# Optimization experiments

Hardware: AMD Instinct MI355X
Metric: run time of the kernel (lower is better)

The kernel has to match this reference:

```python
import jax, jax.numpy as jnp
import numpy as np

N = 40000   # nodes
E = 640000  # edges
D = 128     # hidden_dim
EPS = 1e-5  # LayerNorm eps


def setup_inputs() -> dict:
    key = jax.random.key(0)
    ks = jax.random.split(key, 18)
    s = 0.02
    inp = {
        "h": jax.random.normal(ks[0], (N, D), jnp.float32),
        "x": jax.random.normal(ks[1], (N, 3), jnp.float32),
        "edge_index": jax.random.randint(ks[2], (2, E), 0, N, jnp.int64 if jax.config.jax_enable_x64 else jnp.int32),
        "vel": jax.random.normal(ks[3], (N, 3), jnp.float32),
        # phi_e: Linear(2D+1 -> D), SiLU, Linear(D -> D), SiLU
        "We1": jax.random.normal(ks[4], (2 * D + 1, D), jnp.float32) * s,
        "be1": jnp.zeros((D,), jnp.float32),
        "We2": jax.random.normal(ks[5], (D, D), jnp.float32) * s,
        "be2": jnp.zeros((D,), jnp.float32),
        # phi_x: Linear(D -> D), SiLU, Linear(D -> 1)
        "Wx1": jax.random.normal(ks[6], (D, D), jnp.float32) * s,
        "bx1": jnp.zeros((D,), jnp.float32),
        "Wx2": jax.random.normal(ks[7], (D, 1), jnp.float32) * s,
        "bx2": jnp.zeros((1,), jnp.float32),
        # phi_h: Linear(2D -> D), SiLU, Linear(D -> D)
        "Wh1": jax.random.normal(ks[8], (2 * D, D), jnp.float32) * s,
        "bh1": jnp.zeros((D,), jnp.float32),
        "Wh2": jax.random.normal(ks[9], (D, D), jnp.float32) * s,
        "bh2": jnp.zeros((D,), jnp.float32),
        # LayerNorm
        "gamma": jnp.ones((D,), jnp.float32),
        "beta": jnp.zeros((D,), jnp.float32),
    }
    return inp


def reference(h, x, edge_index, vel,
              We1, be1, We2, be2,
              Wx1, bx1, Wx2, bx2,
              Wh1, bh1, Wh2, bh2,
              gamma, beta):
    src, dst = edge_index[0], edge_index[1]
    rel = x[src] - x[dst]                                  # [E,3]
    dist2 = jnp.sum(rel * rel, axis=-1, keepdims=True)     # [E,1]
    # note: original also computes dist/r_hat and vel[src] but never uses them

    # phi_e on edge features
    e_in = jnp.concatenate([h[src], h[dst], dist2], axis=-1)   # [E,2D+1]
    m = jax.nn.silu(e_in @ We1 + be1)
    m = jax.nn.silu(m @ We2 + be2)                             # [E,D]

    # coordinate update: scatter_mean of rel * phi_x(m) over dst
    coord_w = jax.nn.silu(m @ Wx1 + bx1) @ Wx2 + bx2           # [E,1]
    num = jax.ops.segment_sum(rel * coord_w, dst, num_segments=N)  # [N,3]
    cnt = jax.ops.segment_sum(jnp.ones((E, 1), x.dtype), dst, num_segments=N)
    x_new = x + num / jnp.maximum(cnt, 1.0)

    # node update: scatter_add of messages then phi_h + residual + LayerNorm
    agg = jax.ops.segment_sum(m, dst, num_segments=N)          # [N,D]
    upd = jax.nn.silu(jnp.concatenate([h, agg], axis=-1) @ Wh1 + bh1) @ Wh2 + bh2
    hn = h + upd
    mu = jnp.mean(hn, axis=-1, keepdims=True)
    var = jnp.var(hn, axis=-1, keepdims=True)
    h_out = (hn - mu) / jnp.sqrt(var + EPS) * gamma + beta
    return h_out, x_new
```

## Files before the change

kernel.cpp:

```cpp
#include <hip/hip_runtime.h>
#include <hip/hip_fp16.h>

#define NN 40000
#define NE 640000
#define DD 128
#define NW (NE/64)

typedef _Float16 half8 __attribute__((ext_vector_type(8)));
typedef float f32x4 __attribute__((ext_vector_type(4)));

__device__ __forceinline__ float silu_f(float x){
  return x * __builtin_amdgcn_rcpf(1.f + __expf(-x));
}

__device__ __forceinline__ half8 cvt_h8(float4 a, float4 b){
  half8 r;
  r[0]=(_Float16)a.x; r[1]=(_Float16)a.y; r[2]=(_Float16)a.z; r[3]=(_Float16)a.w;
  r[4]=(_Float16)b.x; r[5]=(_Float16)b.y; r[6]=(_Float16)b.z; r[7]=(_Float16)b.w;
  return r;
}

__device__ __forceinline__ void atom_pk_f16(_Float16* p, unsigned v){
  asm volatile("global_atomic_pk_add_f16 %0, %1, off" :: "v"(p), "v"(v));
}

__global__ void k_hist(const int* __restrict__ ei, int* __restrict__ counts,
                       uint4* __restrict__ aggz){
  int e = blockIdx.x*256 + threadIdx.x;
  if (e < NE){
    atomicAdd(&counts[ei[NE + e]], 1);
    aggz[e] = make_uint4(0,0,0,0);
  }
}

__global__ __launch_bounds__(1024)
void k_scanA(const int* __restrict__ counts, int* __restrict__ woff,
             int* __restrict__ bsum){
  __shared__ int wsum[16];
  const int tid = threadIdx.x, lane = tid & 63, wv = tid >> 6;
  int i = blockIdx.x*1024 + tid;
  int v = (i < NN) ? counts[i] : 0;
  int s = v;
  #pragma unroll
  for (int d = 1; d < 64; d <<= 1){
    int t = __shfl_up(s, d, 64);
    if (lane >= d) s += t;
  }
  if (lane == 63) wsum[wv] = s;
  __syncthreads();
  if (tid < 16){
    int t = wsum[tid];
    #pragma unroll
    for (int d = 1; d < 16; d <<= 1){
      int u = __shfl_up(t, d, 64);
      if (tid >= d) t += u;
    }
    wsum[tid] = t;
  }
  __syncthreads();
  int wbase = (wv == 0) ? 0 : wsum[wv-1];
  if (i < NN) woff[i] = wbase + s - v;
  if (tid == 1023) bsum[blockIdx.x] = wbase + s;
}

__global__ __launch_bounds__(1024)
void k_scanC(int* __restrict__ woff, const int* __restrict__ bsum){
  const int lane = threadIdx.x & 63;
  int v = (lane < 40) ? bsum[lane] : 0;
  int s = v;
  #pragma unroll
  for (int d = 1; d < 64; d <<= 1){
    int t = __shfl_up(s, d, 64);
    if (lane >= d) s += t;
  }
  int boff = (blockIdx.x == 0) ? 0 : __shfl(s, blockIdx.x - 1, 64);
  int i = blockIdx.x*1024 + threadIdx.x;
  if (i < NN) woff[i] += boff;
}

__global__ void k_scatter(const int* __restrict__ ei, int* __restrict__ woff,
                          unsigned* __restrict__ sdp){
  int e = blockIdx.x*256 + threadIdx.x;
  if (e < NE){
    int s = ei[e];
    int d = ei[NE + e];
    int p = atomicAdd(&woff[d], 1);
    sdp[p] = ((unsigned)s << 16) | (unsigned)d;
  }
}

__global__ void k_wt(const float* __restrict__ We1, const float* __restrict__ Wh1,
                     const float* __restrict__ Wh2,
                     _Float16* __restrict__ We1t, _Float16* __restrict__ Wh1t,
                     _Float16* __restrict__ Wh2t, int* __restrict__ counts){
  int i = blockIdx.x*256 + threadIdx.x;
  if (i < 128*256){
    int ch = i >> 8, k = i & 255;
    We1t[i] = (_Float16)We1[k*128 + ch];
    Wh1t[i] = (_Float16)Wh1[k*128 + ch];
  }
  if (i < 128*128){
    int ch = i >> 7, k = i & 127;
    Wh2t[i] = (_Float16)Wh2[k*128 + ch];
  }
  for (int c = i; c < NN; c += 32768) counts[c] = 0;
}

__global__ __launch_bounds__(256) __attribute__((amdgpu_waves_per_eu(3,4)))
void k_gpre(const float* __restrict__ h, const _Float16* __restrict__ We1t,
            const float* __restrict__ be1,
            _Float16* __restrict__ g1, _Float16* __restrict__ g2)
{
  const int tid = threadIdx.x, lane = tid & 63, w = tid >> 6;
  const int q = lane & 15, g = lane >> 4;
  const int base = (blockIdx.x*4 + w) * 16;
  float be1r[8];
  #pragma unroll
  for (int nt=0; nt<8; nt++) be1r[nt] = be1[nt*16+q];

  half8 a[4];
  #pragma unroll
  for (int kk=0; kk<4; kk++){
    const float* rp = h + (size_t)(base+q)*DD + kk*32 + g*8;
    a[kk] = cvt_h8(*(const float4*)rp, *(const float4*)(rp+4));
  }
  f32x4 ac1[8] = {}, ac2[8] = {};
  #pragma unroll
  for (int kk=0; kk<4; kk++){
    #pragma unroll
    for (int nt=0; nt<8; nt++){
      half8 b1 = *(const half8*)&We1t[(nt*16+q)*256 + kk*32 + g*8];
      half8 b2 = *(const half8*)&We1t[(nt*16+q)*256 + 128 + kk*32 + g*8];
      ac1[nt] = __builtin_amdgcn_mfma_f32_16x16x32_f16(a[kk], b1, ac1[nt], 0,0,0);
      ac2[nt] = __builtin_amdgcn_mfma_f32_16x16x32_f16(a[kk], b2, ac2[nt], 0,0,0);
    }
  }
  #pragma unroll
  for (int r=0;r<4;r++){
    int node = base + 4*g + r;
    #pragma unroll
    for (int nt=0; nt<8; nt++){
      g1[(size_t)node*DD + nt*16+q] = (_Float16)(ac1[nt][r] + be1r[nt]);
      g2[(size_t)node*DD + nt*16+q] = (_Float16)ac2[nt][r];
    }
  }
}

__global__ __launch_bounds__(1024) __attribute__((amdgpu_waves_per_eu(4,4)))
void egnn_edge(const _Float16* __restrict__ g1, const _Float16* __restrict__ g2,
               const float* __restrict__ x,
               const unsigned* __restrict__ sdp,
               const float* __restrict__ We1,
               const float* __restrict__ We2, const float* __restrict__ be2,
               const float* __restrict__ Wx1, const float* __restrict__ bx1,
               const float* __restrict__ Wx2, const float* __restrict__ bx2,
               _Float16* __restrict__ agg, float* __restrict__ cwb)
{
  __shared__ __align__(16) _Float16 W2t[128*128];
  __shared__ __align__(16) _Float16 Wxt[128*128];
  __shared__ __align__(16) _Float16 mbuf[16][16*128];
  __shared__ __align__(16) _Float16 w1l_lds[128];

  const int tid = threadIdx.x;
  for (int i = tid; i < 128*128; i += 1024){
    int ch = i & 127, k = i >> 7;
    int sw = (ch & 15) << 3;
    W2t[ch*128 + (k ^ sw)] = (_Float16)We2[k*128 + ch];
    Wxt[ch*128 + (k ^ sw)] = (_Float16)Wx1[k*128 + ch];
  }
  if (tid < 128) w1l_lds[tid] = (_Float16)We1[256*128 + tid];
  const int lane = tid & 63;
  const int w    = tid >> 6;
  const int q    = lane & 15;
  const int g    = lane >> 4;
  float be2r[8], bx1r[8], wx2r[8];
  #pragma unroll
  for (int nt = 0; nt < 8; nt++){
    int ch = nt*16 + q;
    be2r[nt] = be2[ch];
    bx1r[nt] = bx1[ch];
    wx2r[nt] = Wx2[ch];
  }
  const float bx2s = bx2[0];
  _Float16* mb = mbuf[w];
  __syncthreads();

  const int gw = blockIdx.x*16 + w;

  half8 w1l_h[4];
  #pragma unroll
  for (int kk=0; kk<4; kk++)
    w1l_h[kk] = *(const half8*)&w1l_lds[kk*32 + g*8];

  const unsigned sv = sdp[gw*64 + lane];
  const int esrc = (int)(sv >> 16);
  const int edst = (int)(sv & 0xffffu);
  float r0 = x[esrc*3+0] - x[edst*3+0];
  float r1 = x[esrc*3+1] - x[edst*3+1];
  float r2 = x[esrc*3+2] - x[edst*3+2];
  float d2 = r0*r0 + r1*r1 + r2*r2;

  const int first_dst = __shfl(edst, 0, 64);
  const int last_dst  = __shfl(edst, 63, 64);
  const bool prev_spill = (gw > 0)    && ((int)(sdp[gw*64 - 1] & 0xffffu) == first_dst);
  const bool next_spill = (gw < NW-1) && ((int)(sdp[gw*64 + 64] & 0xffffu) == last_dst);

  int srcq[4], dstq[4];
  __half2 d2h[4];
  #pragma unroll
  for (int mt=0; mt<4; mt++){
    srcq[mt] = __shfl(esrc, mt*16 + q, 64);
    dstq[mt] = __shfl(edst, mt*16 + q, 64);
    d2h[mt]  = __float2half2_rn(__shfl(d2, mt*16 + q, 64));
  }
  const __half2 one2 = __float2half2_rn(1.f);

  float fa0 = 0.f, fa1 = 0.f;
  int   fdprev = first_dst;
  bool  seg_first = true;

  uint4 pa1[4], pb1[4];
  #pragma unroll
  for (int kk=0; kk<4; kk++)
    pa1[kk] = *(const uint4*)(g1 + (size_t)srcq[0]*DD + kk*32 + g*8);

  #pragma unroll
  for (int mt=0; mt<4; mt++){
    uint4 (&cu1)[4] = (mt&1) ? pb1 : pa1;
    uint4 (&nu1)[4] = (mt&1) ? pa1 : pb1;
    if (mt < 3){
      #pragma unroll
      for (int kk=0; kk<4; kk++)
        nu1[kk] = *(const uint4*)(g1 + (size_t)srcq[mt+1]*DD + kk*32 + g*8);
    }

    half8 a[4];
    #pragma unroll
    for (int kk=0; kk<4; kk++){
      uint4 cu2 = *(const uint4*)(g2 + (size_t)dstq[mt]*DD + kk*32 + g*8);
      uint4 w4 = __builtin_bit_cast(uint4, w1l_h[kk]);
      unsigned uu1[4] = {cu1[kk].x, cu1[kk].y, cu1[kk].z, cu1[kk].w};
      unsigned uu2[4] = {cu2.x, cu2.y, cu2.z, cu2.w};
      unsigned ww[4]  = {w4.x, w4.y, w4.z, w4.w};
      unsigned zz[4];
      #pragma unroll
      for (int p2=0; p2<4; p2++){
        __half2 z = __hadd2(__builtin_bit_cast(__half2, uu1[p2]),
                            __builtin_bit_cast(__half2, uu2[p2]));
        z = __hfma2(d2h[mt], __builtin_bit_cast(__half2, ww[p2]), z);
        __half2 e   = h2exp(__hneg2(z));
        __half2 den = __hadd2(e, one2);
        __half2 m   = __hmul2(z, h2rcp(den));
        zz[p2] = __builtin_bit_cast(unsigned, m);
      }
      uint4 t; t.x = zz[0]; t.y = zz[1]; t.z = zz[2]; t.w = zz[3];
      a[kk] = __builtin_bit_cast(half8, t);
    }

    f32x4 acc2[8] = {};
    #pragma unroll
    for (int kk=0; kk<4; kk++){
      #pragma unroll
      for (int nt=0; nt<8; nt++){
        half8 b = *(const half8*)&W2t[(nt*16+q)*128 + ((kk*32+g*8) ^ (q<<3))];
        acc2[nt] = __builtin_amdgcn_mfma_f32_16x16x32_f16(a[kk], b, acc2[nt], 0,0,0);
      }
    }
    #pragma unroll
    for (int nt=0; nt<8; nt++){
      #pragma unroll
      for (int r=0;r<4;r++){
        float s = silu_f(acc2[nt][r] + be2r[nt]);
        int el = 4*g + r;
        mb[el*128 + ((nt*16+q) ^ (el<<3))] = (_Float16)s;
      }
    }
    f32x4 acc3[8] = {};
    #pragma unroll
    for (int kk=0; kk<4; kk++){
      half8 am = *(const half8*)&mb[q*128 + ((kk*32+g*8) ^ (q<<3))];
      #pragma unroll
      for (int nt=0; nt<8; nt++){
        half8 b = *(const half8*)&Wxt[(nt*16+q)*128 + ((kk*32+g*8) ^ (q<<3))];
        acc3[nt] = __builtin_amdgcn_mfma_f32_16x16x32_f16(am, b, acc3[nt], 0,0,0);
      }
    }
    float part[4] = {0.f,0.f,0.f,0.f};
    #pragma unroll
    for (int nt=0; nt<8; nt++){
      #pragma unroll
      for (int r=0;r<4;r++)
        part[r] += silu_f(acc3[nt][r] + bx1r[nt]) * wx2r[nt];
    }
    #pragma unroll
    for (int m=1; m<16; m<<=1){
      #pragma unroll
      for (int r=0;r<4;r++) part[r] += __shfl_xor(part[r], m, 64);
    }
    {
      float cw = part[0];
      if (q==1) cw = part[1]; else if (q==2) cw = part[2]; else if (q==3) cw = part[3];
      if (q < 4) cwb[gw*64 + mt*16 + 4*g + q] = cw + bx2s;
    }
    {
      unsigned mv[16];
      #pragma unroll
      for (int e2=0; e2<16; e2++)
        mv[e2] = *(const unsigned*)&mb[e2*128 + ((2*lane) ^ (e2<<3))];
      int dv[16];
      #pragma unroll
      for (int e2=0; e2<16; e2++) dv[e2] = __shfl(edst, mt*16 + e2, 64);
      #pragma unroll
      for (int e2=0; e2<16; e2++){
        if (dv[e2] != fdprev){
          __half2 hv; hv.x = __float2half(fa0); hv.y = __float2half(fa1);
          _Float16* p = agg + (size_t)fdprev*DD + 2*lane;
          if (seg_first && prev_spill) atom_pk_f16(p, __builtin_bit_cast(unsigned, hv));
          else                         *(__half2*)p = hv;
          fa0 = 0.f; fa1 = 0.f; fdprev = dv[e2]; seg_first = false;
        }
        __half2 mvv = __builtin_bit_cast(__half2, mv[e2]);
        fa0 += __half2float(mvv.x);
        fa1 += __half2float(mvv.y);
      }
    }
  }
  {
    __half2 hv; hv.x = __float2half(fa0); hv.y = __float2half(fa1);
    _Float16* p = agg + (size_t)fdprev*DD + 2*lane;
    if ((seg_first && prev_spill) || next_spill) atom_pk_f16(p, __builtin_bit_cast(unsigned, hv));
    else                                         *(__half2*)p = hv;
  }
}

__global__ __launch_bounds__(256) __attribute__((amdgpu_waves_per_eu(3,4)))
void egnn_node(const float* __restrict__ h, const _Float16* __restrict__ agg,
               const _Float16* __restrict__ Wh1t, const _Float16* __restrict__ Wh2t,
               const float* __restrict__ bh1, const float* __restrict__ bh2,
               const float* __restrict__ gam, const float* __restrict__ bet,
               float* __restrict__ hout)
{
  __shared__ __align__(16) _Float16 mbuf[4][16*128];
  const int tid = threadIdx.x, lane = tid & 63, w = tid >> 6;
  const int q = lane & 15, g = lane >> 4;
  const int base = (blockIdx.x*4 + w) * 16;
  float bh1r[8], bh2r[8], gr[8], br[8];
  #pragma unroll
  for (int nt=0; nt<8; nt++){
    int ch = nt*16+q;
    bh1r[nt]=bh1[ch]; bh2r[nt]=bh2[ch]; gr[nt]=gam[ch]; br[nt]=bet[ch];
  }
  _Float16* mb = mbuf[w];

  f32x4 ac1[8] = {};
  #pragma unroll
  for (int kk=0; kk<8; kk++){
    half8 a;
    if (kk < 4){
      const float* rp = h + (size_t)(base+q)*DD + kk*32 + g*8;
      a = cvt_h8(*(const float4*)rp, *(const float4*)(rp+4));
    } else {
      a = *(const half8*)(agg + (size_t)(base+q)*DD + (kk-4)*32 + g*8);
    }
    #pragma unroll
    for (int nt=0; nt<8; nt++){
      half8 b = *(const half8*)&Wh1t[(nt*16+q)*256 + kk*32 + g*8];
      ac1[nt] = __builtin_amdgcn_mfma_f32_16x16x32_f16(a, b, ac1[nt], 0,0,0);
    }
  }
  #pragma unroll
  for (int nt=0; nt<8; nt++){
    #pragma unroll
    for (int r=0;r<4;r++){
      float s = silu_f(ac1[nt][r] + bh1r[nt]);
      int el = 4*g + r;
      mb[el*128 + ((nt*16+q) ^ (el<<3))] = (_Float16)s;
    }
  }
  f32x4 ac2[8] = {};
  #pragma unroll
  for (int kk=0; kk<4; kk++){
    half8 am = *(const half8*)&mb[q*128 + ((kk*32+g*8) ^ (q<<3))];
    #pragma unroll
    for (int nt=0; nt<8; nt++){
      half8 b = *(const half8*)&Wh2t[(nt*16+q)*128 + kk*32 + g*8];
      ac2[nt] = __builtin_amdgcn_mfma_f32_16x16x32_f16(am, b, ac2[nt], 0,0,0);
    }
  }
  #pragma unroll
  for (int r=0;r<4;r++){
    int node = base + 4*g + r;
    float hv[8]; float s1=0.f, s2=0.f;
    #pragma unroll
    for (int nt=0; nt<8; nt++){
      float v = ac2[nt][r] + bh2r[nt] + h[(size_t)node*DD + nt*16 + q];
      hv[nt]=v; s1 += v; s2 += v*v;
    }
    #pragma unroll
    for (int m=1;m<16;m<<=1){ s1 += __shfl_xor(s1,m,64); s2 += __shfl_xor(s2,m,64); }
    float mu  = s1 * (1.f/128.f);
    float var = s2 * (1.f/128.f) - mu*mu;
    float rs  = rsqrtf(var + 1e-5f);
    #pragma unroll
    for (int nt=0; nt<8; nt++)
      hout[(size_t)node*DD + nt*16 + q] = (hv[nt]-mu)*rs*gr[nt] + br[nt];
  }
}

__global__ __launch_bounds__(256)
void k_coord(const float* __restrict__ x, const float* __restrict__ cwb,
             const unsigned* __restrict__ sdp, const int* __restrict__ counts,
             const int* __restrict__ woff, float* __restrict__ xout)
{
  const int tid = threadIdx.x, lane = tid & 63, w = tid >> 6;
  const int sub = lane >> 4, j0 = lane & 15;
  const int n = (blockIdx.x*4 + w)*4 + sub;
  if (n >= NN) return;
  const int cnt = counts[n];
  const int s = woff[n] - cnt;
  float xd0 = x[n*3+0], xd1 = x[n*3+1], xd2 = x[n*3+2];
  float s0=0.f, s1=0.f, s2=0.f;
  for (int j = j0; j < cnt; j += 16){
    int e = s + j;
    float cw = cwb[e];
    int src = (int)(sdp[e] >> 16);
    s0 += (x[src*3+0]-xd0)*cw;
    s1 += (x[src*3+1]-xd1)*cw;
    s2 += (x[src*3+2]-xd2)*cw;
  }
  #pragma unroll
  for (int m=1; m<16; m<<=1){
    s0 += __shfl_xor(s0, m, 64);
    s1 += __shfl_xor(s1, m, 64);
    s2 += __shfl_xor(s2, m, 64);
  }
  if (j0 == 0){
    float inv = __builtin_amdgcn_rcpf((float)(cnt > 1 ? cnt : 1));
    xout[n*3+0] = xd0 + s0*inv;
    xout[n*3+1] = xd1 + s1*inv;
    xout[n*3+2] = xd2 + s2*inv;
  }
}

extern "C" void kernel_launch(void* const* d_in, const int* in_sizes, int n_in,
                              void* d_out, int out_size, void* d_ws, size_t ws_size,
                              hipStream_t stream){
  const float* h   = (const float*)d_in[0];
  const float* x   = (const float*)d_in[1];
  const int*   ei  = (const int*)d_in[2];
  const float* We1 = (const float*)d_in[4];
  const float* be1 = (const float*)d_in[5];
  const float* We2 = (const float*)d_in[6];
  const float* be2 = (const float*)d_in[7];
  const float* Wx1 = (const float*)d_in[8];
  const float* bx1 = (const float*)d_in[9];
  const float* Wx2 = (const float*)d_in[10];
  const float* bx2 = (const float*)d_in[11];
  const float* Wh1 = (const float*)d_in[12];
  const float* bh1 = (const float*)d_in[13];
  const float* Wh2 = (const float*)d_in[14];
  const float* bh2 = (const float*)d_in[15];
  const float* gam = (const float*)d_in[16];
  const float* bet = (const float*)d_in[17];

  float* hout = (float*)d_out;
  float* xout = hout + (size_t)NN*DD;

  char* p = (char*)d_ws;
  _Float16* agg  = (_Float16*)p;  p += (size_t)NN*DD*2;
  _Float16* g1   = (_Float16*)p;  p += (size_t)NN*DD*2;
  _Float16* g2   = (_Float16*)p;  p += (size_t)NN*DD*2;
  int* counts    = (int*)p;       p += (size_t)NN*4;
  int* woff      = (int*)p;       p += (size_t)NN*4;
  unsigned* sdp  = (unsigned*)p;  p += (size_t)NE*4;
  float* cwb     = (float*)p;     p += (size_t)NE*4;
  _Float16* We1t = (_Float16*)p;  p += (size_t)128*256*2;
  _Float16* Wh1t = (_Float16*)p;  p += (size_t)128*256*2;
  _Float16* Wh2t = (_Float16*)p;  p += (size_t)128*128*2;
  int* bsum      = (int*)p;       p += 64*4;

  k_wt<<<128, 256, 0, stream>>>(We1, Wh1, Wh2, We1t, Wh1t, Wh2t, counts);
  k_hist<<<(NE+255)/256, 256, 0, stream>>>(ei, counts, (uint4*)agg);
  k_scanA<<<(NN+1023)/1024, 1024, 0, stream>>>(counts, woff, bsum);
  k_scanC<<<(NN+1023)/1024, 1024, 0, stream>>>(woff, bsum);
  k_scatter<<<(NE+255)/256, 256, 0, stream>>>(ei, woff, sdp);
  k_gpre<<<NN/64, 256, 0, stream>>>(h, We1t, be1, g1, g2);
  egnn_edge<<<NW/16, 1024, 0, stream>>>(g1, g2, x, sdp, We1,
                                        We2, be2, Wx1, bx1, Wx2, bx2,
                                        agg, cwb);
  egnn_node<<<NN/64, 256, 0, stream>>>(h, agg, Wh1t, Wh2t, bh1, bh2,
                                       gam, bet, hout);
  k_coord<<<NN/16, 256, 0, stream>>>(x, cwb, sdp, counts, woff, xout);
}
```

Before: 385.1 us.

## Merge independent kernels into combined launches, resize edge blocks, prefetch g2 rows

Merges the edge scatter kernel with the node pre-projection (k_gpre) into one launch split by block index. It also merges the node update with the coordinate update, since neither depends on the other. The edge kernel goes from 1024-thread blocks to 768-thread blocks with 12 waves and a min-blocks hint of 3, so LDS and occupancy change. It also double-buffers the destination-row (g2) gathers alongside the source-row gathers to hide load latency. The aim is to cut launch gaps and tail idle time, at the cost of more registers in the edge kernel and mixed block types sharing the GPU.

```diff
diff --git a/kernel.cpp b/kernel.cpp
--- a/kernel.cpp
+++ b/kernel.cpp
@@ -76,17 +76,6 @@
   int boff = (blockIdx.x == 0) ? 0 : __shfl(s, blockIdx.x - 1, 64);
   int i = blockIdx.x*1024 + threadIdx.x;
   if (i < NN) woff[i] += boff;
-}
-
-__global__ void k_scatter(const int* __restrict__ ei, int* __restrict__ woff,
-                          unsigned* __restrict__ sdp){
-  int e = blockIdx.x*256 + threadIdx.x;
-  if (e < NE){
-    int s = ei[e];
-    int d = ei[NE + e];
-    int p = atomicAdd(&woff[d], 1);
-    sdp[p] = ((unsigned)s << 16) | (unsigned)d;
-  }
 }
 
 __global__ void k_wt(const float* __restrict__ We1, const float* __restrict__ Wh1,
@@ -106,14 +95,25 @@
   for (int c = i; c < NN; c += 32768) counts[c] = 0;
 }
 
-__global__ __launch_bounds__(256) __attribute__((amdgpu_waves_per_eu(3,4)))
-void k_gpre(const float* __restrict__ h, const _Float16* __restrict__ We1t,
-            const float* __restrict__ be1,
-            _Float16* __restrict__ g1, _Float16* __restrict__ g2)
+__global__ __launch_bounds__(256)
+void k_scatgpre(const int* __restrict__ ei, int* __restrict__ woff,
+                unsigned* __restrict__ sdp,
+                const float* __restrict__ h, const _Float16* __restrict__ We1t,
+                const float* __restrict__ be1,
+                _Float16* __restrict__ g1, _Float16* __restrict__ g2)
 {
+  if (blockIdx.x < NE/256){
+    int e = blockIdx.x*256 + threadIdx.x;
+    int s = ei[e];
+    int d = ei[NE + e];
+    int p = atomicAdd(&woff[d], 1);
+    sdp[p] = ((unsigned)s << 16) | (unsigned)d;
+    return;
+  }
+  const int b = blockIdx.x - NE/256;
   const int tid = threadIdx.x, lane = tid & 63, w = tid >> 6;
   const int q = lane & 15, g = lane >> 4;
-  const int base = (blockIdx.x*4 + w) * 16;
+  const int base = (b*4 + w) * 16;
   float be1r[8];
   #pragma unroll
   for (int nt=0; nt<8; nt++) be1r[nt] = be1[nt*16+q];
@@ -146,7 +146,7 @@
   }
 }
 
-__global__ __launch_bounds__(1024) __attribute__((amdgpu_waves_per_eu(4,4)))
+__global__ __launch_bounds__(768, 3)
 void egnn_edge(const _Float16* __restrict__ g1, const _Float16* __restrict__ g2,
                const float* __restrict__ x,
                const unsigned* __restrict__ sdp,
@@ -158,11 +158,11 @@
 {
   __shared__ __align__(16) _Float16 W2t[128*128];
   __shared__ __align__(16) _Float16 Wxt[128*128];
-  __shared__ __align__(16) _Float16 mbuf[16][16*128];
+  __shared__ __align__(16) _Float16 mbuf[12][16*128];
   __shared__ __align__(16) _Float16 w1l_lds[128];
 
   const int tid = threadIdx.x;
-  for (int i = tid; i < 128*128; i += 1024){
+  for (int i = tid; i < 128*128; i += 768){
     int ch = i & 127, k = i >> 7;
     int sw = (ch & 15) << 3;
     W2t[ch*128 + (k ^ sw)] = (_Float16)We2[k*128 + ch];
@@ -185,7 +185,8 @@
   _Float16* mb = mbuf[w];
   __syncthreads();
 
-  const int gw = blockIdx.x*16 + w;
+  const int gw = blockIdx.x*12 + w;
+  if (gw >= NW) return;
 
   half8 w1l_h[4];
   #pragma unroll
@@ -219,28 +220,33 @@
   int   fdprev = first_dst;
   bool  seg_first = true;
 
-  uint4 pa1[4], pb1[4];
-  #pragma unroll
-  for (int kk=0; kk<4; kk++)
+  uint4 pa1[4], pa2[4], pb1[4], pb2[4];
+  #pragma unroll
+  for (int kk=0; kk<4; kk++){
     pa1[kk] = *(const uint4*)(g1 + (size_t)srcq[0]*DD + kk*32 + g*8);
+    pa2[kk] = *(const uint4*)(g2 + (size_t)dstq[0]*DD + kk*32 + g*8);
+  }
 
   #pragma unroll
   for (int mt=0; mt<4; mt++){
     uint4 (&cu1)[4] = (mt&1) ? pb1 : pa1;
+    uint4 (&cu2)[4] = (mt&1) ? pb2 : pa2;
     uint4 (&nu1)[4] = (mt&1) ? pa1 : pb1;
+    uint4 (&nu2)[4] = (mt&1) ? pa2 : pb2;
     if (mt < 3){
       #pragma unroll
-      for (int kk=0; kk<4; kk++)
+      for (int kk=0; kk<4; kk++){
         nu1[kk] = *(const uint4*)(g1 + (size_t)srcq[mt+1]*DD + kk*32 + g*8);
+        nu2[kk] = *(const uint4*)(g2 + (size_t)dstq[mt+1]*DD + kk*32 + g*8);
+      }
     }
 
     half8 a[4];
     #pragma unroll
     for (int kk=0; kk<4; kk++){
-      uint4 cu2 = *(const uint4*)(g2 + (size_t)dstq[mt]*DD + kk*32 + g*8);
       uint4 w4 = __builtin_bit_cast(uint4, w1l_h[kk]);
       unsigned uu1[4] = {cu1[kk].x, cu1[kk].y, cu1[kk].z, cu1[kk].w};
-      unsigned uu2[4] = {cu2.x, cu2.y, cu2.z, cu2.w};
+      unsigned uu2[4] = {cu2[kk].x, cu2[kk].y, cu2[kk].z, cu2[kk].w};
       unsigned ww[4]  = {w4.x, w4.y, w4.z, w4.w};
       unsigned zz[4];
       #pragma unroll
@@ -333,15 +339,51 @@
   }
 }
 
-__global__ __launch_bounds__(256) __attribute__((amdgpu_waves_per_eu(3,4)))
-void egnn_node(const float* __restrict__ h, const _Float16* __restrict__ agg,
-               const _Float16* __restrict__ Wh1t, const _Float16* __restrict__ Wh2t,
-               const float* __restrict__ bh1, const float* __restrict__ bh2,
-               const float* __restrict__ gam, const float* __restrict__ bet,
-               float* __restrict__ hout)
+__global__ __launch_bounds__(256)
+void k_nodecoord(const float* __restrict__ h, const _Float16* __restrict__ agg,
+                 const _Float16* __restrict__ Wh1t, const _Float16* __restrict__ Wh2t,
+                 const float* __restrict__ bh1, const float* __restrict__ bh2,
+                 const float* __restrict__ gam, const float* __restrict__ bet,
+                 const float* __restrict__ x, const float* __restrict__ cwb,
+                 const unsigned* __restrict__ sdp, const int* __restrict__ counts,
+                 const int* __restrict__ woff,
+                 float* __restrict__ hout, float* __restrict__ xout)
 {
   __shared__ __align__(16) _Float16 mbuf[4][16*128];
   const int tid = threadIdx.x, lane = tid & 63, w = tid >> 6;
+
+  if (blockIdx.x >= NN/64){
+    const int bidx = blockIdx.x - NN/64;
+    const int sub = lane >> 4, j0 = lane & 15;
+    const int n = (bidx*4 + w)*4 + sub;
+    if (n >= NN) return;
+    const int cnt = counts[n];
+    const int s = woff[n] - cnt;
+    float xd0 = x[n*3+0], xd1 = x[n*3+1], xd2 = x[n*3+2];
+    float s0=0.f, s1=0.f, s2=0.f;
+    for (int j = j0; j < cnt; j += 16){
+      int e = s + j;
+      float cw = cwb[e];
+      int src = (int)(sdp[e] >> 16);
+      s0 += (x[src*3+0]-xd0)*cw;
+      s1 += (x[src*3+1]-xd1)*cw;
+      s2 += (x[src*3+2]-xd2)*cw;
+    }
+    #pragma unroll
+    for (int m=1; m<16; m<<=1){
+      s0 += __shfl_xor(s0, m, 64);
+      s1 += __shfl_xor(s1, m, 64);
+      s2 += __shfl_xor(s2, m, 64);
+    }
+    if (j0 == 0){
+      float inv = __builtin_amdgcn_rcpf((float)(cnt > 1 ? cnt : 1));
+      xout[n*3+0] = xd0 + s0*inv;
+      xout[n*3+1] = xd1 + s1*inv;
+      xout[n*3+2] = xd2 + s2*inv;
+    }
+    return;
+  }
+
   const int q = lane & 15, g = lane >> 4;
   const int base = (blockIdx.x*4 + w) * 16;
   float bh1r[8], bh2r[8], gr[8], br[8];
@@ -404,41 +446,6 @@
     #pragma unroll
     for (int nt=0; nt<8; nt++)
       hout[(size_t)node*DD + nt*16 + q] = (hv[nt]-mu)*rs*gr[nt] + br[nt];
-  }
-}
-
-__global__ __launch_bounds__(256)
-void k_coord(const float* __restrict__ x, const float* __restrict__ cwb,
-             const unsigned* __restrict__ sdp, const int* __restrict__ counts,
-             const int* __restrict__ woff, float* __restrict__ xout)
-{
-  const int tid = threadIdx.x, lane = tid & 63, w = tid >> 6;
-  const int sub = lane >> 4, j0 = lane & 15;
-  const int n = (blockIdx.x*4 + w)*4 + sub;
-  if (n >= NN) return;
-  const int cnt = counts[n];
-  const int s = woff[n] - cnt;
-  float xd0 = x[n*3+0], xd1 = x[n*3+1], xd2 = x[n*3+2];
-  float s0=0.f, s1=0.f, s2=0.f;
-  for (int j = j0; j < cnt; j += 16){
-    int e = s + j;
-    float cw = cwb[e];
-    int src = (int)(sdp[e] >> 16);
-    s0 += (x[src*3+0]-xd0)*cw;
-    s1 += (x[src*3+1]-xd1)*cw;
-    s2 += (x[src*3+2]-xd2)*cw;
-  }
-  #pragma unroll
-  for (int m=1; m<16; m<<=1){
-    s0 += __shfl_xor(s0, m, 64);
-    s1 += __shfl_xor(s1, m, 64);
-    s2 += __shfl_xor(s2, m, 64);
-  }
-  if (j0 == 0){
-    float inv = __builtin_amdgcn_rcpf((float)(cnt > 1 ? cnt : 1));
-    xout[n*3+0] = xd0 + s0*inv;
-    xout[n*3+1] = xd1 + s1*inv;
-    xout[n*3+2] = xd2 + s2*inv;
   }
 }
 
@@ -483,12 +490,11 @@
   k_hist<<<(NE+255)/256, 256, 0, stream>>>(ei, counts, (uint4*)agg);
   k_scanA<<<(NN+1023)/1024, 1024, 0, stream>>>(counts, woff, bsum);
   k_scanC<<<(NN+1023)/1024, 1024, 0, stream>>>(woff, bsum);
-  k_scatter<<<(NE+255)/256, 256, 0, stream>>>(ei, woff, sdp);
-  k_gpre<<<NN/64, 256, 0, stream>>>(h, We1t, be1, g1, g2);
-  egnn_edge<<<NW/16, 1024, 0, stream>>>(g1, g2, x, sdp, We1,
-                                        We2, be2, Wx1, bx1, Wx2, bx2,
-                                        agg, cwb);
-  egnn_node<<<NN/64, 256, 0, stream>>>(h, agg, Wh1t, Wh2t, bh1, bh2,
-                                       gam, bet, hout);
-  k_coord<<<NN/16, 256, 0, stream>>>(x, cwb, sdp, counts, woff, xout);
-}
+  k_scatgpre<<<NE/256 + NN/64, 256, 0, stream>>>(ei, woff, sdp, h, We1t, be1, g1, g2);
+  egnn_edge<<<(NW + 11)/12, 768, 0, stream>>>(g1, g2, x, sdp, We1,
+                                              We2, be2, Wx1, bx1, Wx2, bx2,
+                                              agg, cwb);
+  k_nodecoord<<<NN/64 + NN/16, 256, 0, stream>>>(h, agg, Wh1t, Wh2t, bh1, bh2,
+                                                 gam, bet, x, cwb, sdp, counts,
+                                                 woff, hout, xout);
+}
```

After: 332.8 us (median of 3 runs). -13.6%, faster.
